# Kernel tuning notes

Measured on AMD Instinct MI355X. Metric: run time of the kernel, lower is better.

## Reference

```python
import jax, jax.numpy as jnp
import numpy as np

K = 20          # neighbors
EPS = 1e-5      # BatchNorm eps
SLOPE = 0.2     # LeakyReLU negative slope


def setup_inputs() -> dict:
    key = jax.random.key(0)
    ks = jax.random.split(key, 6)
    B, C, N, O = 8, 3, 4096, 64
    x = jax.random.normal(ks[0], (B, C, N), dtype=jnp.float32)
    W = jax.random.normal(ks[1], (O, 2 * C), dtype=jnp.float32) * 0.1  # conv1x1 weight, bias=False
    gamma = 1.0 + 0.1 * jax.random.normal(ks[2], (O,), dtype=jnp.float32)
    beta = 0.1 * jax.random.normal(ks[3], (O,), dtype=jnp.float32)
    mean = 0.1 * jax.random.normal(ks[4], (O,), dtype=jnp.float32)
    var = jax.random.uniform(ks[5], (O,), dtype=jnp.float32, minval=0.5, maxval=1.5)
    return {"x": x, "W": W, "gamma": gamma, "beta": beta, "mean": mean, "var": var}


def reference(x, W, gamma, beta, mean, var):
    # x: [B, C, N]
    B, C, N = x.shape
    xt = jnp.swapaxes(x, 1, 2)                                   # [B, N, C]
    xx = jnp.sum(x * x, axis=1)                                  # [B, N]
    pd = 2.0 * jnp.einsum('bnc,bmc->bnm', xt, xt) - xx[:, :, None] - xx[:, None, :]
    _, idx = jax.lax.top_k(pd, K)                                # [B, N, K] nearest neighbors
    # gather neighbor features per batch
    feat = jax.vmap(lambda f, i: f[i])(xt, idx)                  # [B, N, K, C]
    center = xt[:, :, None, :]                                   # [B, N, 1, C]
    edge = jnp.concatenate(
        [feat - center, jnp.broadcast_to(center, feat.shape)], axis=-1)  # [B, N, K, 2C]
    # 1x1 conv == channel matmul
    y = jnp.einsum('bnkc,oc->bnko', edge, W)                     # [B, N, K, O]
    inv = gamma / jnp.sqrt(var + EPS)                            # fused inference BatchNorm
    y = y * inv + (beta - mean * inv)
    y = jnp.where(y >= 0, y, SLOPE * y)                          # LeakyReLU(0.2)
    y = jnp.max(y, axis=2)                                       # max over k -> [B, N, O]
    return jnp.swapaxes(y, 1, 2)                                 # [B, O, N]
```

## Files before the change

kernel.cpp:

```cpp
#include <hip/hip_runtime.h>
#include <math.h>

#define NPTS 4096
#define KNN  20
#define NOUT 64
#define WPB  2
#define QPW  4
#define QBLK (WPB * QPW)
#define BLKT (WPB * 64)
#define PCAP 128
#define MITER 8

__device__ __forceinline__ unsigned ord32(float f) {
    unsigned u = __float_as_uint(f);
    int m = ((int)u) >> 31;
    return u ^ ((unsigned)m | 0x80000000u);
}
__device__ __forceinline__ float iord32(unsigned r) {
    unsigned u = (r & 0x80000000u) ? (r ^ 0x80000000u) : ~r;
    return __uint_as_float(u);
}
__device__ __forceinline__ int mbcnt64(unsigned long long m) {
    return __builtin_amdgcn_mbcnt_hi((unsigned)(m >> 32),
           __builtin_amdgcn_mbcnt_lo((unsigned)m, 0));
}

__global__ __launch_bounds__(256) void pack_kernel(const float* __restrict__ x,
                                                   float4* __restrict__ xq) {
    const int i = blockIdx.x * 256 + threadIdx.x;
    const int b = i >> 12, j = i & (NPTS - 1);
    const float* xb = x + (size_t)b * 3 * NPTS;
    const float a0 = xb[j], a1 = xb[NPTS + j], a2 = xb[2 * NPTS + j];
    xq[i] = make_float4(a0, a1, a2, -fmaf(a0, a0, fmaf(a1, a1, a2 * a2)));
}

__global__ __launch_bounds__(BLKT, 8) void edgeconv_kernel(
    const float4* __restrict__ xq,
    const float* __restrict__ Wm,
    const float* __restrict__ gamma,
    const float* __restrict__ beta,
    const float* __restrict__ mean,
    const float* __restrict__ var,
    float* __restrict__ out)
{
    const int bid = blockIdx.x;
    const int b   = bid >> 9;
    const int n0  = (bid & 511) * QBLK;
    const int t    = threadIdx.x;
    const int lane = t & 63;
    const int w    = t >> 6;

    __shared__ unsigned long long pool[QBLK * PCAP];
    __shared__ int cnt[QBLK];

    const float4* xqb = xq + (size_t)b * NPTS;

    if (lane < QPW) cnt[QPW * w + lane] = 0;

    const int na = __builtin_amdgcn_readfirstlane(n0 + QPW * w);
    float q0[QPW], q1[QPW], q2[QPW];
    #pragma unroll
    for (int q = 0; q < QPW; ++q) {
        const float4 pv = xqb[na + q];
        q0[q] = 2.f * pv.x; q1[q] = 2.f * pv.y; q2[q] = 2.f * pv.z;
    }

    float vm0[QPW], vm1[QPW];
    #pragma unroll
    for (int q = 0; q < QPW; ++q) { vm0[q] = -INFINITY; vm1[q] = -INFINITY; }
    #pragma unroll
    for (int g = 0; g < MITER; ++g) {
        float4 cc[4];
        #pragma unroll
        for (int u = 0; u < 4; ++u) cc[u] = xqb[(g * 4 + u) * 64 + lane];
        #pragma unroll
        for (int u = 0; u < 4; ++u) {
            #pragma unroll
            for (int q = 0; q < QPW; ++q) {
                const float e = fmaf(q0[q], cc[u].x, fmaf(q1[q], cc[u].y, fmaf(q2[q], cc[u].z, cc[u].w)));
                if (g < MITER / 2) vm0[q] = fmaxf(vm0[q], e);
                else               vm1[q] = fmaxf(vm1[q], e);
            }
        }
    }

    float Tf[QPW];
    #pragma unroll
    for (int q = 0; q < QPW; ++q) {
        const unsigned h0 = ord32(vm0[q]) >> 16;
        const unsigned h1 = ord32(vm1[q]) >> 16;
        unsigned K = 0;
        #pragma unroll
        for (int bit = 15; bit >= 0; --bit) {
            const unsigned p = K | (1u << bit);
            const int c = __popcll(__ballot(h0 >= p)) + __popcll(__ballot(h1 >= p));
            if (c >= KNN) K = p;
        }
        Tf[q] = iord32(K << 16);
    }

    const int invl = (NPTS - 1) - lane;

    #pragma unroll
    for (int g = 0; g < NPTS / 256; ++g) {
        float4 cc[4];
        #pragma unroll
        for (int u = 0; u < 4; ++u) cc[u] = xqb[(g * 4 + u) * 64 + lane];
        #pragma unroll
        for (int u = 0; u < 4; ++u) {
            const unsigned tag = (unsigned)(invl - (g * 4 + u) * 64);
            #pragma unroll
            for (int q = 0; q < QPW; ++q) {
                const float e = fmaf(q0[q], cc[u].x, fmaf(q1[q], cc[u].y, fmaf(q2[q], cc[u].z, cc[u].w)));
                if (e >= Tf[q]) {
                    const int pos = atomicAdd(&cnt[QPW * w + q], 1);
                    if (pos < PCAP)
                        pool[(QPW * w + q) * PCAP + pos] =
                            ((unsigned long long)ord32(e) << 32) | tag;
                }
            }
        }
    }

    unsigned myidx[QPW];
    #pragma unroll
    for (int q = 0; q < QPW; ++q) {
        const int pr = QPW * w + q;
        unsigned long long* pl = pool + (size_t)pr * PCAP;
        int cw = __builtin_amdgcn_readfirstlane(cnt[pr]);
        if (cw > PCAP) cw = PCAP;

        const unsigned long long e0 = (lane < cw) ? pl[lane] : 0ull;
        const unsigned long long e1 = (lane + 64 < cw) ? pl[lane + 64] : 0ull;
        const unsigned k0 = (unsigned)(e0 >> 32), t0 = (unsigned)e0;
        const unsigned k1 = (unsigned)(e1 >> 32), t1 = (unsigned)e1;

        unsigned K = 0;
        #pragma unroll
        for (int bit = 31; bit >= 0; --bit) {
            const unsigned p = K | (1u << bit);
            const int c = __popcll(__ballot(k0 >= p)) + __popcll(__ballot(k1 >= p));
            if (c >= KNN) K = p;
        }

        unsigned long long g0 = __ballot(k0 > K);
        unsigned long long g1 = __ballot(k1 > K);
        const int m = __popcll(g0) + __popcll(g1);
        unsigned long long s0 = __ballot(k0 == K);
        unsigned long long s1 = __ballot(k1 == K);
        const int r = KNN - m;
        if (__popcll(s0) + __popcll(s1) > r) {
            unsigned TT = 0;
            #pragma unroll
            for (int bit = 11; bit >= 0; --bit) {
                const unsigned p = TT | (1u << bit);
                const int c = __popcll(__ballot(k0 == K && t0 >= p)) +
                              __popcll(__ballot(k1 == K && t1 >= p));
                if (c >= r) TT = p;
            }
            s0 = __ballot(k0 == K && t0 >= TT);
            s1 = __ballot(k1 == K && t1 >= TT);
        }

        unsigned* idxq = (unsigned*)pl;
        if ((g0 >> lane) & 1) idxq[mbcnt64(g0)] = t0;
        if ((g1 >> lane) & 1) idxq[__popcll(g0) + mbcnt64(g1)] = t1;
        if ((s0 >> lane) & 1) idxq[m + mbcnt64(s0)] = t0;
        if ((s1 >> lane) & 1) idxq[m + __popcll(s0) + mbcnt64(s1)] = t1;
        myidx[q] = idxq[(lane < KNN) ? lane : 0];
    }

    const int o = lane;
    const float iv   = gamma[o] / sqrtf(var[o] + 1e-5f);
    const float bias = beta[o] - mean[o] * iv;
    const float* Wr = Wm + o * 6;
    const float w0p = Wr[0] * iv, w1p = Wr[1] * iv, w2p = Wr[2] * iv;
    const float w3p = Wr[3] * iv, w4p = Wr[4] * iv, w5p = Wr[5] * iv;

    float bests[QPW];
    #pragma unroll
    for (int q = 0; q < QPW; ++q) {
        const float4 pv = xqb[na + q];
        const float basep = fmaf(w3p, pv.x, fmaf(w4p, pv.y, fmaf(w5p, pv.z, bias)));
        const float base2 = basep - fmaf(w0p, pv.x, fmaf(w1p, pv.y, w2p * pv.z));
        float best = -INFINITY;
        #pragma unroll
        for (int k = 0; k < KNN; ++k) {
            const int lk = __builtin_amdgcn_readlane((int)myidx[q], k);
            const int gi = __builtin_amdgcn_readfirstlane((NPTS - 1) - lk);
            const float4 f = xqb[gi];
            float y = fmaf(w0p, f.x, fmaf(w1p, f.y, fmaf(w2p, f.z, base2)));
            y = fmaxf(y, 0.2f * y);
            best = fmaxf(best, y);
        }
        bests[q] = best;
    }

    float4 res;
    res.x = bests[0]; res.y = bests[1]; res.z = bests[2]; res.w = bests[3];
    *(float4*)(out + ((size_t)b * NOUT + o) * NPTS + na) = res;
}

extern "C" void kernel_launch(void* const* d_in, const int* in_sizes, int n_in,
                              void* d_out, int out_size, void* d_ws, size_t ws_size,
                              hipStream_t stream) {
    const float* x     = (const float*)d_in[0];
    const float* Wm    = (const float*)d_in[1];
    const float* gamma = (const float*)d_in[2];
    const float* beta  = (const float*)d_in[3];
    const float* mean  = (const float*)d_in[4];
    const float* var   = (const float*)d_in[5];
    float* out = (float*)d_out;
    float4* xq = (float4*)d_ws;

    const int B = in_sizes[0] / (3 * NPTS);
    pack_kernel<<<B * NPTS / 256, 256, 0, stream>>>(x, xq);
    const int nblocks = B * (NPTS / QBLK);
    edgeconv_kernel<<<nblocks, BLKT, 0, stream>>>(xq, Wm, gamma, beta, mean, var, out);
}
```

Before: 125.5 us.

## Replace LDS atomic candidate append with wave ballot compaction and interleave per-query selection

Candidate insertion into the per-query LDS pool now uses a wave-wide ballot plus mbcnt prefix to compute slots, with the counters held in registers. This removes the shared-memory atomicAdd and the counter array. The radix-threshold searches now run for all four queries together inside a single non-unrolled bit loop, and most loops are switched to unroll 1 to shrink code size and register pressure. Risks are extra ballot work per candidate group and more loop overhead from the reduced unrolling.

```diff
diff --git a/kernel.cpp b/kernel.cpp
--- a/kernel.cpp
+++ b/kernel.cpp
@@ -51,11 +51,8 @@
     const int w    = t >> 6;
 
     __shared__ unsigned long long pool[QBLK * PCAP];
-    __shared__ int cnt[QBLK];
 
     const float4* xqb = xq + (size_t)b * NPTS;
-
-    if (lane < QPW) cnt[QPW * w + lane] = 0;
 
     const int na = __builtin_amdgcn_readfirstlane(n0 + QPW * w);
     float q0[QPW], q1[QPW], q2[QPW];
@@ -68,8 +65,9 @@
     float vm0[QPW], vm1[QPW];
     #pragma unroll
     for (int q = 0; q < QPW; ++q) { vm0[q] = -INFINITY; vm1[q] = -INFINITY; }
-    #pragma unroll
-    for (int g = 0; g < MITER; ++g) {
+
+    #pragma unroll 1
+    for (int g = 0; g < MITER / 2; ++g) {
         float4 cc[4];
         #pragma unroll
         for (int u = 0; u < 4; ++u) cc[u] = xqb[(g * 4 + u) * 64 + lane];
@@ -78,30 +76,49 @@
             #pragma unroll
             for (int q = 0; q < QPW; ++q) {
                 const float e = fmaf(q0[q], cc[u].x, fmaf(q1[q], cc[u].y, fmaf(q2[q], cc[u].z, cc[u].w)));
-                if (g < MITER / 2) vm0[q] = fmaxf(vm0[q], e);
-                else               vm1[q] = fmaxf(vm1[q], e);
-            }
-        }
-    }
-
+                vm0[q] = fmaxf(vm0[q], e);
+            }
+        }
+    }
+    #pragma unroll 1
+    for (int g = MITER / 2; g < MITER; ++g) {
+        float4 cc[4];
+        #pragma unroll
+        for (int u = 0; u < 4; ++u) cc[u] = xqb[(g * 4 + u) * 64 + lane];
+        #pragma unroll
+        for (int u = 0; u < 4; ++u) {
+            #pragma unroll
+            for (int q = 0; q < QPW; ++q) {
+                const float e = fmaf(q0[q], cc[u].x, fmaf(q1[q], cc[u].y, fmaf(q2[q], cc[u].z, cc[u].w)));
+                vm1[q] = fmaxf(vm1[q], e);
+            }
+        }
+    }
+
+    unsigned h0[QPW], h1[QPW], Kq[QPW];
+    #pragma unroll
+    for (int q = 0; q < QPW; ++q) {
+        h0[q] = ord32(vm0[q]) >> 16;
+        h1[q] = ord32(vm1[q]) >> 16;
+        Kq[q] = 0;
+    }
+    #pragma unroll 1
+    for (int bit = 15; bit >= 0; --bit) {
+        #pragma unroll
+        for (int q = 0; q < QPW; ++q) {
+            const unsigned p = Kq[q] | (1u << bit);
+            const int c = __popcll(__ballot(h0[q] >= p)) + __popcll(__ballot(h1[q] >= p));
+            if (c >= KNN) Kq[q] = p;
+        }
+    }
     float Tf[QPW];
     #pragma unroll
-    for (int q = 0; q < QPW; ++q) {
-        const unsigned h0 = ord32(vm0[q]) >> 16;
-        const unsigned h1 = ord32(vm1[q]) >> 16;
-        unsigned K = 0;
-        #pragma unroll
-        for (int bit = 15; bit >= 0; --bit) {
-            const unsigned p = K | (1u << bit);
-            const int c = __popcll(__ballot(h0 >= p)) + __popcll(__ballot(h1 >= p));
-            if (c >= KNN) K = p;
-        }
-        Tf[q] = iord32(K << 16);
-    }
+    for (int q = 0; q < QPW; ++q) Tf[q] = iord32(Kq[q] << 16);
 
     const int invl = (NPTS - 1) - lane;
 
-    #pragma unroll
+    int cq0 = 0, cq1 = 0, cq2 = 0, cq3 = 0;
+    #pragma unroll 1
     for (int g = 0; g < NPTS / 256; ++g) {
         float4 cc[4];
         #pragma unroll
@@ -109,64 +126,74 @@
         #pragma unroll
         for (int u = 0; u < 4; ++u) {
             const unsigned tag = (unsigned)(invl - (g * 4 + u) * 64);
+            float e4[QPW];
+            #pragma unroll
+            for (int q = 0; q < QPW; ++q)
+                e4[q] = fmaf(q0[q], cc[u].x, fmaf(q1[q], cc[u].y, fmaf(q2[q], cc[u].z, cc[u].w)));
             #pragma unroll
             for (int q = 0; q < QPW; ++q) {
-                const float e = fmaf(q0[q], cc[u].x, fmaf(q1[q], cc[u].y, fmaf(q2[q], cc[u].z, cc[u].w)));
-                if (e >= Tf[q]) {
-                    const int pos = atomicAdd(&cnt[QPW * w + q], 1);
-                    if (pos < PCAP)
+                const unsigned long long mask = __ballot(e4[q] >= Tf[q]);
+                int* cqp = (q == 0) ? &cq0 : (q == 1) ? &cq1 : (q == 2) ? &cq2 : &cq3;
+                if (mask) {
+                    const int pos = *cqp + mbcnt64(mask);
+                    if (((mask >> lane) & 1) && pos < PCAP)
                         pool[(QPW * w + q) * PCAP + pos] =
-                            ((unsigned long long)ord32(e) << 32) | tag;
+                            ((unsigned long long)ord32(e4[q]) << 32) | tag;
+                    *cqp += __popcll(mask);
                 }
             }
         }
     }
 
-    unsigned myidx[QPW];
-    #pragma unroll
-    for (int q = 0; q < QPW; ++q) {
-        const int pr = QPW * w + q;
-        unsigned long long* pl = pool + (size_t)pr * PCAP;
-        int cw = __builtin_amdgcn_readfirstlane(cnt[pr]);
-        if (cw > PCAP) cw = PCAP;
-
+    unsigned k0[QPW], k1[QPW], t0v[QPW], t1v[QPW], Ks[QPW];
+    int cqa[QPW] = {cq0, cq1, cq2, cq3};
+    #pragma unroll
+    for (int q = 0; q < QPW; ++q) {
+        int cw = cqa[q]; if (cw > PCAP) cw = PCAP;
+        const unsigned long long* pl = pool + (size_t)(QPW * w + q) * PCAP;
         const unsigned long long e0 = (lane < cw) ? pl[lane] : 0ull;
         const unsigned long long e1 = (lane + 64 < cw) ? pl[lane + 64] : 0ull;
-        const unsigned k0 = (unsigned)(e0 >> 32), t0 = (unsigned)e0;
-        const unsigned k1 = (unsigned)(e1 >> 32), t1 = (unsigned)e1;
-
-        unsigned K = 0;
-        #pragma unroll
-        for (int bit = 31; bit >= 0; --bit) {
-            const unsigned p = K | (1u << bit);
-            const int c = __popcll(__ballot(k0 >= p)) + __popcll(__ballot(k1 >= p));
-            if (c >= KNN) K = p;
-        }
-
-        unsigned long long g0 = __ballot(k0 > K);
-        unsigned long long g1 = __ballot(k1 > K);
+        k0[q] = (unsigned)(e0 >> 32); t0v[q] = (unsigned)e0;
+        k1[q] = (unsigned)(e1 >> 32); t1v[q] = (unsigned)e1;
+        Ks[q] = 0;
+    }
+    #pragma unroll 1
+    for (int bit = 31; bit >= 0; --bit) {
+        #pragma unroll
+        for (int q = 0; q < QPW; ++q) {
+            const unsigned p = Ks[q] | (1u << bit);
+            const int c = __popcll(__ballot(k0[q] >= p)) + __popcll(__ballot(k1[q] >= p));
+            if (c >= KNN) Ks[q] = p;
+        }
+    }
+
+    unsigned myidx[QPW];
+    #pragma unroll
+    for (int q = 0; q < QPW; ++q) {
+        unsigned long long g0 = __ballot(k0[q] > Ks[q]);
+        unsigned long long g1 = __ballot(k1[q] > Ks[q]);
         const int m = __popcll(g0) + __popcll(g1);
-        unsigned long long s0 = __ballot(k0 == K);
-        unsigned long long s1 = __ballot(k1 == K);
+        unsigned long long s0 = __ballot(k0[q] == Ks[q]);
+        unsigned long long s1 = __ballot(k1[q] == Ks[q]);
         const int r = KNN - m;
         if (__popcll(s0) + __popcll(s1) > r) {
             unsigned TT = 0;
-            #pragma unroll
+            #pragma unroll 1
             for (int bit = 11; bit >= 0; --bit) {
                 const unsigned p = TT | (1u << bit);
-                const int c = __popcll(__ballot(k0 == K && t0 >= p)) +
-                              __popcll(__ballot(k1 == K && t1 >= p));
+                const int c = __popcll(__ballot(k0[q] == Ks[q] && t0v[q] >= p)) +
+                              __popcll(__ballot(k1[q] == Ks[q] && t1v[q] >= p));
                 if (c >= r) TT = p;
             }
-            s0 = __ballot(k0 == K && t0 >= TT);
-            s1 = __ballot(k1 == K && t1 >= TT);
-        }
-
-        unsigned* idxq = (unsigned*)pl;
-        if ((g0 >> lane) & 1) idxq[mbcnt64(g0)] = t0;
-        if ((g1 >> lane) & 1) idxq[__popcll(g0) + mbcnt64(g1)] = t1;
-        if ((s0 >> lane) & 1) idxq[m + mbcnt64(s0)] = t0;
-        if ((s1 >> lane) & 1) idxq[m + __popcll(s0) + mbcnt64(s1)] = t1;
+            s0 = __ballot(k0[q] == Ks[q] && t0v[q] >= TT);
+            s1 = __ballot(k1[q] == Ks[q] && t1v[q] >= TT);
+        }
+
+        unsigned* idxq = (unsigned*)(pool + (size_t)(QPW * w + q) * PCAP);
+        if ((g0 >> lane) & 1) idxq[mbcnt64(g0)] = t0v[q];
+        if ((g1 >> lane) & 1) idxq[__popcll(g0) + mbcnt64(g1)] = t1v[q];
+        if ((s0 >> lane) & 1) idxq[m + mbcnt64(s0)] = t0v[q];
+        if ((s1 >> lane) & 1) idxq[m + __popcll(s0) + mbcnt64(s1)] = t1v[q];
         myidx[q] = idxq[(lane < KNN) ? lane : 0];
     }
 
@@ -184,14 +211,21 @@
         const float basep = fmaf(w3p, pv.x, fmaf(w4p, pv.y, fmaf(w5p, pv.z, bias)));
         const float base2 = basep - fmaf(w0p, pv.x, fmaf(w1p, pv.y, w2p * pv.z));
         float best = -INFINITY;
-        #pragma unroll
-        for (int k = 0; k < KNN; ++k) {
-            const int lk = __builtin_amdgcn_readlane((int)myidx[q], k);
-            const int gi = __builtin_amdgcn_readfirstlane((NPTS - 1) - lk);
-            const float4 f = xqb[gi];
-            float y = fmaf(w0p, f.x, fmaf(w1p, f.y, fmaf(w2p, f.z, base2)));
-            y = fmaxf(y, 0.2f * y);
-            best = fmaxf(best, y);
+        #pragma unroll 1
+        for (int kc = 0; kc < KNN; kc += 4) {
+            float4 f[4];
+            #pragma unroll
+            for (int j = 0; j < 4; ++j) {
+                const int lk = __builtin_amdgcn_readlane((int)myidx[q], kc + j);
+                const int gi = __builtin_amdgcn_readfirstlane((NPTS - 1) - lk);
+                f[j] = xqb[gi];
+            }
+            #pragma unroll
+            for (int j = 0; j < 4; ++j) {
+                float y = fmaf(w0p, f[j].x, fmaf(w1p, f[j].y, fmaf(w2p, f[j].z, base2)));
+                y = fmaxf(y, 0.2f * y);
+                best = fmaxf(best, y);
+            }
         }
         bests[q] = best;
     }
```

Result: slower. 130.0 us (+3.6%).

## Pack points in pairs and use packed FP32 FMA for distance scans

Applied to the files above, without the earlier changes.

Repacks the point workspace into a pair-interleaved SoA layout (x0,x1,y0,y1 / z0,z1,w0,w1) so each lane handles two candidate points per iteration. The distance computation then uses two-wide packed FMA and max (v_pk_fma_f32-style), roughly halving the VALU instruction count of both the threshold-estimation and candidate-collection scans. The final gather has to select between odd and even elements with two loads per neighbor, and launch bounds drop from 8 to 6 waves to allow more registers. The threshold-estimation sample stays at 2048 points, now covered in half the iterations.

```diff
diff --git a/kernel.cpp b/kernel.cpp
--- a/kernel.cpp
+++ b/kernel.cpp
@@ -9,7 +9,9 @@
 #define QBLK (WPB * QPW)
 #define BLKT (WPB * 64)
 #define PCAP 128
-#define MITER 8
+#define NPAIR (NPTS / 2)
+
+typedef float f32x2 __attribute__((ext_vector_type(2)));
 
 __device__ __forceinline__ unsigned ord32(float f) {
     unsigned u = __float_as_uint(f);
@@ -24,17 +26,26 @@
     return __builtin_amdgcn_mbcnt_hi((unsigned)(m >> 32),
            __builtin_amdgcn_mbcnt_lo((unsigned)m, 0));
 }
+__device__ __forceinline__ f32x2 pkfma(f32x2 a, f32x2 b, f32x2 c) {
+    return __builtin_elementwise_fma(a, b, c);
+}
 
 __global__ __launch_bounds__(256) void pack_kernel(const float* __restrict__ x,
                                                    float4* __restrict__ xq) {
     const int i = blockIdx.x * 256 + threadIdx.x;
-    const int b = i >> 12, j = i & (NPTS - 1);
+    const int b = i >> 11, j = i & (NPAIR - 1);
     const float* xb = x + (size_t)b * 3 * NPTS;
-    const float a0 = xb[j], a1 = xb[NPTS + j], a2 = xb[2 * NPTS + j];
-    xq[i] = make_float4(a0, a1, a2, -fmaf(a0, a0, fmaf(a1, a1, a2 * a2)));
-}
-
-__global__ __launch_bounds__(BLKT, 8) void edgeconv_kernel(
+    const f32x2 xx = *(const f32x2*)(xb + 2 * j);
+    const f32x2 yy = *(const f32x2*)(xb + NPTS + 2 * j);
+    const f32x2 zz = *(const f32x2*)(xb + 2 * NPTS + 2 * j);
+    const float w0 = -fmaf(xx.x, xx.x, fmaf(yy.x, yy.x, zz.x * zz.x));
+    const float w1 = -fmaf(xx.y, xx.y, fmaf(yy.y, yy.y, zz.y * zz.y));
+    float4* dst = xq + (size_t)b * (2 * NPAIR);
+    dst[j]         = make_float4(xx.x, xx.y, yy.x, yy.y);
+    dst[NPAIR + j] = make_float4(zz.x, zz.y, w0, w1);
+}
+
+__global__ __launch_bounds__(BLKT, 6) void edgeconv_kernel(
     const float4* __restrict__ xq,
     const float* __restrict__ Wm,
     const float* __restrict__ gamma,
@@ -53,33 +64,48 @@
     __shared__ unsigned long long pool[QBLK * PCAP];
     __shared__ int cnt[QBLK];
 
-    const float4* xqb = xq + (size_t)b * NPTS;
+    const float4* Ab = xq + (size_t)b * (2 * NPAIR);
+    const float4* Bb = Ab + NPAIR;
 
     if (lane < QPW) cnt[QPW * w + lane] = 0;
 
     const int na = __builtin_amdgcn_readfirstlane(n0 + QPW * w);
-    float q0[QPW], q1[QPW], q2[QPW];
-    #pragma unroll
-    for (int q = 0; q < QPW; ++q) {
-        const float4 pv = xqb[na + q];
-        q0[q] = 2.f * pv.x; q1[q] = 2.f * pv.y; q2[q] = 2.f * pv.z;
-    }
-
-    float vm0[QPW], vm1[QPW];
-    #pragma unroll
-    for (int q = 0; q < QPW; ++q) { vm0[q] = -INFINITY; vm1[q] = -INFINITY; }
-    #pragma unroll
-    for (int g = 0; g < MITER; ++g) {
-        float4 cc[4];
-        #pragma unroll
-        for (int u = 0; u < 4; ++u) cc[u] = xqb[(g * 4 + u) * 64 + lane];
-        #pragma unroll
-        for (int u = 0; u < 4; ++u) {
+    const float4 A0 = Ab[na / 2], A1 = Ab[na / 2 + 1];
+    const float4 B0 = Bb[na / 2], B1 = Bb[na / 2 + 1];
+    const float q0s[QPW] = {2.f * A0.x, 2.f * A0.y, 2.f * A1.x, 2.f * A1.y};
+    const float q1s[QPW] = {2.f * A0.z, 2.f * A0.w, 2.f * A1.z, 2.f * A1.w};
+    const float q2s[QPW] = {2.f * B0.x, 2.f * B0.y, 2.f * B1.x, 2.f * B1.y};
+    f32x2 Q0[QPW], Q1[QPW], Q2[QPW];
+    #pragma unroll
+    for (int q = 0; q < QPW; ++q) {
+        Q0[q] = (f32x2){q0s[q], q0s[q]};
+        Q1[q] = (f32x2){q1s[q], q1s[q]};
+        Q2[q] = (f32x2){q2s[q], q2s[q]};
+    }
+
+    f32x2 vm0[QPW], vm1[QPW];
+    #pragma unroll
+    for (int q = 0; q < QPW; ++q) {
+        vm0[q] = (f32x2){-INFINITY, -INFINITY};
+        vm1[q] = (f32x2){-INFINITY, -INFINITY};
+    }
+    #pragma unroll
+    for (int g = 0; g < 4; ++g) {
+        float4 av[4], bv[4];
+        #pragma unroll
+        for (int u = 0; u < 4; ++u) {
+            const int pi = (g * 4 + u) * 64 + lane;
+            av[u] = Ab[pi]; bv[u] = Bb[pi];
+        }
+        #pragma unroll
+        for (int u = 0; u < 4; ++u) {
+            const f32x2 X = {av[u].x, av[u].y}, Y = {av[u].z, av[u].w};
+            const f32x2 Z = {bv[u].x, bv[u].y}, Wp = {bv[u].z, bv[u].w};
             #pragma unroll
             for (int q = 0; q < QPW; ++q) {
-                const float e = fmaf(q0[q], cc[u].x, fmaf(q1[q], cc[u].y, fmaf(q2[q], cc[u].z, cc[u].w)));
-                if (g < MITER / 2) vm0[q] = fmaxf(vm0[q], e);
-                else               vm1[q] = fmaxf(vm1[q], e);
+                const f32x2 e2 = pkfma(Q0[q], X, pkfma(Q1[q], Y, pkfma(Q2[q], Z, Wp)));
+                if (g < 2) vm0[q] = __builtin_elementwise_max(vm0[q], e2);
+                else       vm1[q] = __builtin_elementwise_max(vm1[q], e2);
             }
         }
     }
@@ -87,8 +113,8 @@
     float Tf[QPW];
     #pragma unroll
     for (int q = 0; q < QPW; ++q) {
-        const unsigned h0 = ord32(vm0[q]) >> 16;
-        const unsigned h1 = ord32(vm1[q]) >> 16;
+        const unsigned h0 = ord32(fmaxf(vm0[q].x, vm0[q].y)) >> 16;
+        const unsigned h1 = ord32(fmaxf(vm1[q].x, vm1[q].y)) >> 16;
         unsigned K = 0;
         #pragma unroll
         for (int bit = 15; bit >= 0; --bit) {
@@ -99,24 +125,36 @@
         Tf[q] = iord32(K << 16);
     }
 
-    const int invl = (NPTS - 1) - lane;
-
-    #pragma unroll
-    for (int g = 0; g < NPTS / 256; ++g) {
-        float4 cc[4];
-        #pragma unroll
-        for (int u = 0; u < 4; ++u) cc[u] = xqb[(g * 4 + u) * 64 + lane];
-        #pragma unroll
-        for (int u = 0; u < 4; ++u) {
-            const unsigned tag = (unsigned)(invl - (g * 4 + u) * 64);
+    const int lane2 = 2 * lane;
+
+    #pragma unroll
+    for (int g = 0; g < 8; ++g) {
+        float4 av[4], bv[4];
+        #pragma unroll
+        for (int u = 0; u < 4; ++u) {
+            const int pi = (g * 4 + u) * 64 + lane;
+            av[u] = Ab[pi]; bv[u] = Bb[pi];
+        }
+        #pragma unroll
+        for (int u = 0; u < 4; ++u) {
+            const f32x2 X = {av[u].x, av[u].y}, Y = {av[u].z, av[u].w};
+            const f32x2 Z = {bv[u].x, bv[u].y}, Wp = {bv[u].z, bv[u].w};
+            const int tb = (NPTS - 1) - 2 * ((g * 4 + u) * 64);
+            const unsigned tag0 = (unsigned)(tb - lane2);
             #pragma unroll
             for (int q = 0; q < QPW; ++q) {
-                const float e = fmaf(q0[q], cc[u].x, fmaf(q1[q], cc[u].y, fmaf(q2[q], cc[u].z, cc[u].w)));
-                if (e >= Tf[q]) {
+                const f32x2 e2 = pkfma(Q0[q], X, pkfma(Q1[q], Y, pkfma(Q2[q], Z, Wp)));
+                if (e2.x >= Tf[q]) {
                     const int pos = atomicAdd(&cnt[QPW * w + q], 1);
                     if (pos < PCAP)
                         pool[(QPW * w + q) * PCAP + pos] =
-                            ((unsigned long long)ord32(e) << 32) | tag;
+                            ((unsigned long long)ord32(e2.x) << 32) | tag0;
+                }
+                if (e2.y >= Tf[q]) {
+                    const int pos = atomicAdd(&cnt[QPW * w + q], 1);
+                    if (pos < PCAP)
+                        pool[(QPW * w + q) * PCAP + pos] =
+                            ((unsigned long long)ord32(e2.y) << 32) | (tag0 - 1);
                 }
             }
         }
@@ -177,19 +215,27 @@
     const float w0p = Wr[0] * iv, w1p = Wr[1] * iv, w2p = Wr[2] * iv;
     const float w3p = Wr[3] * iv, w4p = Wr[4] * iv, w5p = Wr[5] * iv;
 
+    const float pvx[QPW] = {A0.x, A0.y, A1.x, A1.y};
+    const float pvy[QPW] = {A0.z, A0.w, A1.z, A1.w};
+    const float pvz[QPW] = {B0.x, B0.y, B1.x, B1.y};
+
     float bests[QPW];
     #pragma unroll
     for (int q = 0; q < QPW; ++q) {
-        const float4 pv = xqb[na + q];
-        const float basep = fmaf(w3p, pv.x, fmaf(w4p, pv.y, fmaf(w5p, pv.z, bias)));
-        const float base2 = basep - fmaf(w0p, pv.x, fmaf(w1p, pv.y, w2p * pv.z));
+        const float basep = fmaf(w3p, pvx[q], fmaf(w4p, pvy[q], fmaf(w5p, pvz[q], bias)));
+        const float base2 = basep - fmaf(w0p, pvx[q], fmaf(w1p, pvy[q], w2p * pvz[q]));
         float best = -INFINITY;
         #pragma unroll
         for (int k = 0; k < KNN; ++k) {
             const int lk = __builtin_amdgcn_readlane((int)myidx[q], k);
             const int gi = __builtin_amdgcn_readfirstlane((NPTS - 1) - lk);
-            const float4 f = xqb[gi];
-            float y = fmaf(w0p, f.x, fmaf(w1p, f.y, fmaf(w2p, f.z, base2)));
+            const int pair = gi >> 1, odd = gi & 1;
+            const float4 fa = Ab[pair];
+            const f32x2  fz = *(const f32x2*)(Bb + pair);
+            const float fx = odd ? fa.y : fa.x;
+            const float fy = odd ? fa.w : fa.z;
+            const float fzz = odd ? fz.y : fz.x;
+            float y = fmaf(w0p, fx, fmaf(w1p, fy, fmaf(w2p, fzz, base2)));
             y = fmaxf(y, 0.2f * y);
             best = fmaxf(best, y);
         }
@@ -214,7 +260,7 @@
     float4* xq = (float4*)d_ws;
 
     const int B = in_sizes[0] / (3 * NPTS);
-    pack_kernel<<<B * NPTS / 256, 256, 0, stream>>>(x, xq);
+    pack_kernel<<<B * NPAIR / 256, 256, 0, stream>>>(x, xq);
     const int nblocks = B * (NPTS / QBLK);
     edgeconv_kernel<<<nblocks, BLKT, 0, stream>>>(xq, Wm, gamma, beta, mean, var, out);
 }
```

Measured after the change: 173.6 us. 38.4% more time.
